# Kernel tuning notes

Measured on AMD Instinct MI355X. Metric: run time of the kernel, lower is better.

Reference implementation:

```python
import math
import jax, jax.numpy as jnp
import numpy as np

B, T = 2, 2048
D_MODEL, D_HEAD = 2048, 128
N_Q, N_KV = 16, 4
QPG = N_Q // N_KV  # queries per kv group
ROPE_BASE = 10000.0
YARN_SCALE = 4.0
ORIG_MAX_LEN = 4096
BETA_FAST, BETA_SLOW = 32.0, 1.0
RMS_EPS = 1.1920929e-07  # torch.finfo(float32).eps (nn.RMSNorm default)


def _yarn_inv_freq():
    inv = 1.0 / ROPE_BASE ** (np.arange(0, D_HEAD, 2, dtype=np.float32) / D_HEAD)
    wavelengths = 2.0 * math.pi / inv
    low_wavelen = ORIG_MAX_LEN / BETA_SLOW
    high_wavelen = ORIG_MAX_LEN / BETA_FAST
    gamma = np.clip((low_wavelen - wavelengths) / (low_wavelen - high_wavelen), 0.0, 1.0)
    return (gamma * inv + (1.0 - gamma) * inv / YARN_SCALE).astype(np.float32)

INV_FREQ = jnp.asarray(_yarn_inv_freq())  # (D_HEAD//2,) constant buffer
MSCALE = 0.1 * math.log(YARN_SCALE) + 1.0
ATTN_SCALE = 1.0 / (MSCALE * math.sqrt(D_HEAD))


def _rms_norm(x, w):
    # normalize over last dim (d_head), learnable per-dim weight
    return x * jax.lax.rsqrt(jnp.mean(x * x, axis=-1, keepdims=True) + RMS_EPS) * w


def _apply_rope(x):
    # x: (..., T, d_head)
    t = jnp.arange(x.shape[-2], dtype=jnp.float32)
    freqs = jnp.outer(t, INV_FREQ)                 # (T, d/2)
    emb = jnp.concatenate([freqs, freqs], axis=-1)  # (T, d)
    cos, sin = jnp.cos(emb), jnp.sin(emb)
    half = x.shape[-1] // 2
    x_rot = jnp.concatenate([-x[..., half:], x[..., :half]], axis=-1)
    return x * cos + x_rot * sin


def setup_inputs() -> dict:
    key = jax.random.key(0)
    ks = jax.random.split(key, 5)
    x = jax.random.normal(ks[0], (B, T, D_MODEL), dtype=jnp.float32)
    w_scale = 0.02
    Wq = jax.random.normal(ks[1], (D_MODEL, N_Q * D_HEAD), dtype=jnp.float32) * w_scale
    Wkv = jax.random.normal(ks[2], (D_MODEL, 2 * N_KV * D_HEAD), dtype=jnp.float32) * w_scale
    Wo = jax.random.normal(ks[3], (N_Q * D_HEAD, D_MODEL), dtype=jnp.float32) * w_scale
    q_norm_w = jnp.ones((D_HEAD,), dtype=jnp.float32)
    k_norm_w = jnp.ones((D_HEAD,), dtype=jnp.float32)
    return {"x": x, "Wq": Wq, "Wkv": Wkv, "Wo": Wo,
            "q_norm_w": q_norm_w, "k_norm_w": k_norm_w}


def reference(x, Wq, Wkv, Wo, q_norm_w, k_norm_w):
    b, t, _ = x.shape
    # projections
    q = (x @ Wq).reshape(b, t, QPG, N_KV, D_HEAD).transpose(0, 2, 3, 1, 4)  # (b,qpg,g,t,d)
    kv = x @ Wkv
    k, v = jnp.split(kv, 2, axis=-1)
    k = k.reshape(b, t, N_KV, D_HEAD).transpose(0, 2, 1, 3)  # (b,g,t,d)
    v = v.reshape(b, t, N_KV, D_HEAD).transpose(0, 2, 1, 3)  # (b,g,t,d)
    # RMSNorm + YaRN RoPE on q,k (math done in float32 as in source)
    q = _apply_rope(_rms_norm(q, q_norm_w))
    k = _apply_rope(_rms_norm(k, k_norm_w))
    # GQA replication: head index h = qpg*N_KV + g (matches source rearrange/reshape)
    q = q.reshape(b, N_Q, t, D_HEAD)
    k = jnp.broadcast_to(k[:, None], (b, QPG, N_KV, t, D_HEAD)).reshape(b, N_Q, t, D_HEAD)
    v = jnp.broadcast_to(v[:, None], (b, QPG, N_KV, t, D_HEAD)).reshape(b, N_Q, t, D_HEAD)
    # causal SDPA with custom scale
    scores = jnp.einsum('bhtd,bhsd->bhts', q, k) * ATTN_SCALE
    causal = jnp.tril(jnp.ones((t, t), dtype=bool))
    scores = jnp.where(causal, scores, jnp.finfo(scores.dtype).min)
    probs = jax.nn.softmax(scores, axis=-1)
    attn = jnp.einsum('bhts,bhsd->bhtd', probs, v)
    out = attn.transpose(0, 2, 1, 3).reshape(b, t, N_Q * D_HEAD)
    return out @ Wo
```

## Files before the change

kernel.cpp:

```cpp
#include <hip/hip_runtime.h>
#include <cmath>

typedef float f32x4 __attribute__((ext_vector_type(4)));
typedef __bf16 bf16x8 __attribute__((ext_vector_type(8)));

#define DEV static __device__ __forceinline__

DEV unsigned short f2bf(float f) {
  unsigned int u = __builtin_bit_cast(unsigned int, f);
  u += 0x7FFFu + ((u >> 16) & 1u);
  return (unsigned short)(u >> 16);
}
DEV float bf2f(unsigned short h) {
  unsigned int u = ((unsigned int)h) << 16;
  return __builtin_bit_cast(float, u);
}
DEV unsigned int cvtpk(float lo, float hi) {
  unsigned int r;
  asm("v_cvt_pk_bf16_f32 %0, %1, %2" : "=v"(r) : "v"(lo), "v"(hi));
  return r;
}
DEV f32x4 mfma16(bf16x8 a, bf16x8 b, f32x4 c) {
  return __builtin_amdgcn_mfma_f32_16x16x32_bf16(a, b, c, 0, 0, 0);
}
DEV void dma16(const void* g, void* l) {
  __builtin_amdgcn_global_load_lds(
      (const __attribute__((address_space(1))) void*)(uintptr_t)g,
      (__attribute__((address_space(3))) void*)(unsigned int)(uintptr_t)l,
      16, 0, 0);
}

constexpr int T_SEQ = 2048;

__global__ __launch_bounds__(256) void prep_all(const float4* __restrict__ in,
                                                ushort* __restrict__ out,
                                                float2* __restrict__ rope,
                                                const float* __restrict__ Wq,
                                                const float* __restrict__ Wkv,
                                                const float* __restrict__ Wo,
                                                ushort* __restrict__ wqkv,
                                                ushort* __restrict__ wot) {
  __shared__ ushort tile[64][65];
  const int bx = blockIdx.x;
  if (bx < 8192) {
    int i = bx * 256 + threadIdx.x;
    float4 v = in[i];
    unsigned int lo = (unsigned int)f2bf(v.x) | ((unsigned int)f2bf(v.y) << 16);
    unsigned int hi = (unsigned int)f2bf(v.z) | ((unsigned int)f2bf(v.w) << 16);
    int row = i >> 9;
    int e = (i * 4) & 2047;
    size_t o = ((size_t)row << 11) + (size_t)(e ^ ((row & 7) << 3));
    *(uint2*)(out + o) = make_uint2(lo, hi);
  } else if (bx < 8704) {
    int gid = (bx - 8192) * 256 + threadIdx.x;
    int t = gid >> 6, i = gid & 63;
    double inv = pow(10000.0, -((double)(2 * i)) / 128.0);
    double wl = 6.283185307179586 / inv;
    double gm = (4096.0 - wl) / (4096.0 - 128.0);
    gm = gm < 0.0 ? 0.0 : (gm > 1.0 ? 1.0 : gm);
    float f = (float)(gm * inv + (1.0 - gm) * inv * 0.25);
    float th = (float)t * f;
    float s, c;
    sincosf(th, &s, &c);
    rope[gid] = make_float2(c, s);
  } else {
    const int l = bx - 8704;
    const int bxl0 = l % 80, by = l / 80;
    const float* src;
    ushort* dst;
    int C, bxl;
    if (bxl0 < 32) {
      src = Wq; dst = wqkv; C = 2048; bxl = bxl0;
    } else if (bxl0 < 48) {
      src = Wkv; dst = wqkv + (size_t)2048 * 2048; C = 1024; bxl = bxl0 - 32;
    } else {
      src = Wo; dst = wot; C = 2048; bxl = bxl0 - 48;
    }
    const int R = 2048;
    int c0 = bxl * 64, r0 = by * 64;
    int j = threadIdx.x & 63, i0 = threadIdx.x >> 6;
#pragma unroll
    for (int ii = 0; ii < 16; ++ii) {
      int i = i0 + ii * 4;
      tile[i][j] = f2bf(src[(size_t)(r0 + i) * C + c0 + j]);
    }
    __syncthreads();
#pragma unroll
    for (int ii = 0; ii < 16; ++ii) {
      int jr = i0 + ii * 4;
      dst[(size_t)(c0 + jr) * R + ((r0 + j) ^ ((jr & 7) << 3))] = tile[j][jr];
    }
  }
}

template <int BM, int BN, int OUT_BF16>
__global__ __launch_bounds__(512) void gemm256(const ushort* __restrict__ A,
                                               const ushort* __restrict__ Bt,
                                               void* __restrict__ Cv,
                                               int M, int N, int K) {
  constexpr int MT = BM / 32;
  constexpr int NT = BN / 64;
  constexpr int NPH = (MT / 4) * (NT / 2);
  constexpr int ADMA = BM / 64;
  constexpr int BDMA = BN / 64;
  __shared__ ushort lA[2][BM * 64];
  __shared__ ushort lB[2][BN * 64];
  const int tid = threadIdx.x, lane = tid & 63, w = tid >> 6;
  const int wm = (w >> 2) * (BM / 2);
  const int wn = (w & 3) * (BN / 4);
  const int m0 = blockIdx.y * BM, n0 = blockIdx.x * BN;

  f32x4 acc[MT][NT] = {};

  const size_t K2 = (size_t)K * 2;
  const char* Ab = (const char*)A + (size_t)m0 * K2;
  const char* Bb = (const char*)Bt + (size_t)n0 * K2;
  const int srb = lane >> 3;
  const int scb = (lane & 7) * 16;

  auto stage = [&](int t, int bi) {
#pragma unroll
    for (int ii = 0; ii < ADMA; ++ii) {
      const int ar = w * (BM / 8) + ii * 8;
      dma16(Ab + (size_t)(ar + srb) * K2 + (size_t)t * 128 + scb,
            (char*)lA[bi] + ar * 128);
    }
#pragma unroll
    for (int ii = 0; ii < BDMA; ++ii) {
      const int br = w * (BN / 8) + ii * 8;
      dma16(Bb + (size_t)(br + srb) * K2 + (size_t)t * 128 + scb,
            (char*)lB[bi] + br * 128);
    }
  };

  stage(0, 0);
  const int nkt = K >> 6;

  for (int t = 0; t < nkt; ++t) {
    const int cur = t & 1;
    if (t + 1 < nkt) {
      stage(t + 1, cur ^ 1);
      if constexpr (ADMA + BDMA == 8)
        asm volatile("s_waitcnt vmcnt(8)" ::: "memory");
      else if constexpr (ADMA + BDMA == 6)
        asm volatile("s_waitcnt vmcnt(6)" ::: "memory");
      else
        asm volatile("s_waitcnt vmcnt(4)" ::: "memory");
    } else {
      asm volatile("s_waitcnt vmcnt(0)" ::: "memory");
    }
    __builtin_amdgcn_s_barrier();
    __builtin_amdgcn_sched_barrier(0);

    const char* lAc = (const char*)lA[cur];
    const char* lBc = (const char*)lB[cur];

#pragma unroll
    for (int ph = 0; ph < NPH; ++ph) {
      const int mb = (ph / (NT / 2)) * 4;
      const int nb = (ph % (NT / 2)) * 2;
#pragma unroll
      for (int kk = 0; kk < 2; ++kk) {
        bf16x8 af[4], bfr[2];
        const int byo = kk * 64 + ((lane >> 4) << 4);
#pragma unroll
        for (int i = 0; i < 4; ++i) {
          int row = wm + (mb + i) * 16 + (lane & 15);
          af[i] = *(const bf16x8*)(lAc + row * 128 + (byo ^ ((row & 7) << 4)));
        }
#pragma unroll
        for (int i = 0; i < 2; ++i) {
          int row = wn + (nb + i) * 16 + (lane & 15);
          bfr[i] = *(const bf16x8*)(lBc + row * 128 + (byo ^ ((row & 7) << 4)));
        }
        __builtin_amdgcn_s_setprio(1);
#pragma unroll
        for (int i = 0; i < 4; ++i)
#pragma unroll
          for (int j = 0; j < 2; ++j)
            acc[mb + i][nb + j] = mfma16(af[i], bfr[j], acc[mb + i][nb + j]);
        __builtin_amdgcn_s_setprio(0);
      }
    }
    __builtin_amdgcn_sched_barrier(0);
    __builtin_amdgcn_s_barrier();
  }

  const int rr = (lane >> 4) << 2;
  const int cc = lane & 15;
  if (OUT_BF16) {
    ushort* C = (ushort*)Cv;
#pragma unroll
    for (int mt = 0; mt < MT; ++mt)
#pragma unroll
      for (int nt = 0; nt < NT; ++nt)
#pragma unroll
        for (int j = 0; j < 4; ++j) {
          int r = m0 + wm + mt * 16 + rr + j;
          int c = n0 + wn + nt * 16 + cc;
          C[(size_t)r * N + c] = f2bf(acc[mt][nt][j]);
        }
  } else {
    float* C = (float*)Cv;
#pragma unroll
    for (int mt = 0; mt < MT; ++mt)
#pragma unroll
      for (int nt = 0; nt < NT; ++nt)
#pragma unroll
        for (int j = 0; j < 4; ++j) {
          int r = m0 + wm + mt * 16 + rr + j;
          int c = n0 + wn + nt * 16 + cc;
          C[(size_t)r * N + c] = acc[mt][nt][j];
        }
  }
}

__global__ __launch_bounds__(256) void normrope_tv(const ushort* __restrict__ qkv,
                                                   const float* __restrict__ qw,
                                                   const float* __restrict__ kw,
                                                   const float2* __restrict__ rope,
                                                   ushort* __restrict__ qout,
                                                   ushort* __restrict__ kout,
                                                   ushort* __restrict__ vt,
                                                   float q_scale) {
  __shared__ ushort tile[64][65];
  const int bx = blockIdx.x;
  if (bx < 20480) {
    const int w = threadIdx.x >> 6, lane = threadIdx.x & 63;
    const int vi = bx * 4 + w;
    const ushort* src;
    const float* wt;
    ushort* dst;
    float extra;
    int t, bb;
    if (vi < 65536) {
      int row = vi >> 4, H = vi & 15;
      bb = row >> 11;
      t = row & 2047;
      src = qkv + (size_t)row * 3072 + H * 128 + lane * 2;
      wt = qw;
      extra = q_scale;
      dst = qout + ((size_t)(bb * 16 + H) * T_SEQ + t) * 128 + lane * 2;
    } else {
      int vi2 = vi - 65536;
      int row = vi2 >> 2, gg = vi2 & 3;
      bb = row >> 11;
      t = row & 2047;
      src = qkv + (size_t)row * 3072 + 2048 + gg * 128 + lane * 2;
      wt = kw;
      extra = 1.f;
      dst = kout + ((size_t)(bb * 4 + gg) * T_SEQ + t) * 128 +
            ((lane * 2) ^ ((t & 7) << 3));
    }
    float x0 = bf2f(src[0]), x1 = bf2f(src[1]);
    float ss = x0 * x0 + x1 * x1;
#pragma unroll
    for (int d = 1; d < 64; d <<= 1) ss += __shfl_xor(ss, d, 64);
    float sc = rsqrtf(ss * (1.f / 128.f) + 1.1920929e-7f);
    float w0 = wt[lane * 2], w1 = wt[lane * 2 + 1];
    float xn0 = x0 * sc * w0, xn1 = x1 * sc * w1;
    float p0 = __shfl_xor(xn0, 32, 64), p1 = __shfl_xor(xn1, 32, 64);
    float r0 = lane < 32 ? -p0 : p0;
    float r1 = lane < 32 ? -p1 : p1;
    int i0 = (lane * 2) & 63;
    float2 cs0 = rope[t * 64 + i0];
    float2 cs1 = rope[t * 64 + i0 + 1];
    float o0 = (xn0 * cs0.x + r0 * cs0.y) * extra;
    float o1 = (xn1 * cs1.x + r1 * cs1.y) * extra;
    unsigned int pkv = (unsigned int)f2bf(o0) | ((unsigned int)f2bf(o1) << 16);
    *(unsigned int*)dst = pkv;
  } else {
    const int l = bx - 20480;
    int t0 = (l & 31) * 64;
    int y = l >> 5;
    int dh = y & 1, bg = y >> 1;
    int bb = bg >> 2, g = bg & 3;
    int j = threadIdx.x & 63, i0 = threadIdx.x >> 6;
#pragma unroll
    for (int ii = 0; ii < 16; ++ii) {
      int i = i0 + ii * 4;
      tile[i][j] = qkv[(size_t)(bb * T_SEQ + t0 + i) * 3072 + 2560 + g * 128 + dh * 64 + j];
    }
    __syncthreads();
#pragma unroll
    for (int ii = 0; ii < 16; ++ii) {
      int jr = i0 + ii * 4;
      vt[((size_t)bg * 128 + dh * 64 + jr) * T_SEQ + ((t0 + j) ^ ((jr & 7) << 3))] = tile[j][jr];
    }
  }
}

__global__ __launch_bounds__(256, 2) void attn_fwd(const ushort* __restrict__ qh,
                                                   const ushort* __restrict__ kh,
                                                   const ushort* __restrict__ vt,
                                                   ushort* __restrict__ o) {
  const int f = blockIdx.x;
  const int half = f >> 8, c = f & 255;
  const int kk = c >> 5, bh = c & 31;
  const int qt = half ? kk : (15 - kk);
  const int b = bh >> 4, H = bh & 15;
  const int g = H & 3;
  const int tid = threadIdx.x, lane = tid & 63, w = tid >> 6;
  const int wrow0 = qt * 128 + w * 32;

  __shared__ ushort lK[2][64 * 128];
  __shared__ ushort lV[2][128 * 64];
  __shared__ ushort lP[4 * 32 * 64];

  bf16x8 qf[2][4];
#pragma unroll
  for (int mt = 0; mt < 2; ++mt) {
    const ushort* qb = qh + ((size_t)(b * 16 + H) * T_SEQ + wrow0 + mt * 16 + (lane & 15)) * 128 +
                       ((lane >> 4) << 3);
#pragma unroll
    for (int kc = 0; kc < 4; ++kc) qf[mt][kc] = *(const bf16x8*)(qb + kc * 32);
  }

  f32x4 oacc[2][8] = {};
  float mrow[2] = {-INFINITY, -INFINITY};
  float lrow[2] = {0.f, 0.f};

  const char* kpl = (const char*)(kh + (size_t)(b * 4 + g) * T_SEQ * 128);
  const char* vpl = (const char*)(vt + (size_t)(b * 4 + g) * 128 * T_SEQ);

  auto stage = [&](int j, int bi) {
#pragma unroll
    for (int ii = 0; ii < 4; ++ii) {
      const int off = w * 4096 + ii * 1024;
      dma16(kpl + (size_t)j * 16384 + off + lane * 16, (char*)lK[bi] + off);
      const int vrow = w * 32 + ii * 8 + (lane >> 3);
      dma16(vpl + (size_t)vrow * (T_SEQ * 2) + j * 128 + (lane & 7) * 16,
            (char*)lV[bi] + off);
    }
  };

  stage(0, 0);

  const int rsel = ((lane >> 4) << 2);

  const int jmax = 2 * qt + 1;
  for (int j = 0; j <= jmax; ++j) {
    const int cur = j & 1;
    if (j < jmax) {
      stage(j + 1, cur ^ 1);
      asm volatile("s_waitcnt vmcnt(8)" ::: "memory");
    } else {
      asm volatile("s_waitcnt vmcnt(0)" ::: "memory");
    }
    __builtin_amdgcn_s_barrier();
    __builtin_amdgcn_sched_barrier(0);

    f32x4 s[2][4];
#pragma unroll
    for (int nt = 0; nt < 4; ++nt) {
      bf16x8 kf[4];
      int krow = nt * 16 + (lane & 15);
#pragma unroll
      for (int kc = 0; kc < 4; ++kc) {
        int byo = kc * 64 + ((lane >> 4) << 4);
        kf[kc] = *(const bf16x8*)((const char*)lK[cur] + krow * 256 + (byo ^ ((krow & 7) << 4)));
      }
#pragma unroll
      for (int mt = 0; mt < 2; ++mt) {
        f32x4 a = {0.f, 0.f, 0.f, 0.f};
#pragma unroll
        for (int kc = 0; kc < 4; ++kc) a = mfma16(kf[kc], qf[mt][kc], a);
        s[mt][nt] = a;
      }
    }

    if (j * 64 + 63 > wrow0) {
#pragma unroll
      for (int mt = 0; mt < 2; ++mt) {
        int qrow = wrow0 + mt * 16 + (lane & 15);
#pragma unroll
        for (int nt = 0; nt < 4; ++nt)
#pragma unroll
          for (int jj = 0; jj < 4; ++jj) {
            int col = j * 64 + nt * 16 + rsel + jj;
            if (col > qrow) s[mt][nt][jj] = -3.0e38f;
          }
      }
    }

    float pmx[2], mn[2];
#pragma unroll
    for (int mt = 0; mt < 2; ++mt) {
      float a0 = fmaxf(fmaxf(s[mt][0][0], s[mt][0][1]), fmaxf(s[mt][0][2], s[mt][0][3]));
      float a1 = fmaxf(fmaxf(s[mt][1][0], s[mt][1][1]), fmaxf(s[mt][1][2], s[mt][1][3]));
      float a2 = fmaxf(fmaxf(s[mt][2][0], s[mt][2][1]), fmaxf(s[mt][2][2], s[mt][2][3]));
      float a3 = fmaxf(fmaxf(s[mt][3][0], s[mt][3][1]), fmaxf(s[mt][3][2], s[mt][3][3]));
      float p = fmaxf(fmaxf(a0, a1), fmaxf(a2, a3));
      p = fmaxf(p, __shfl_xor(p, 16, 64));
      p = fmaxf(p, __shfl_xor(p, 32, 64));
      pmx[mt] = p;
      mn[mt] = mrow[mt];
    }

    bool ok = (pmx[0] <= mrow[0] + 11.5417f) && (pmx[1] <= mrow[1] + 11.5417f);
    if (!__all(ok)) {
#pragma unroll
      for (int mt = 0; mt < 2; ++mt) {
        mn[mt] = fmaxf(mrow[mt], pmx[mt]);
        float rsc = exp2f(mrow[mt] - mn[mt]);
        mrow[mt] = mn[mt];
        lrow[mt] *= rsc;
        float rr0 = __shfl(rsc, rsel + 0, 64);
        float rr1 = __shfl(rsc, rsel + 1, 64);
        float rr2 = __shfl(rsc, rsel + 2, 64);
        float rr3 = __shfl(rsc, rsel + 3, 64);
#pragma unroll
        for (int dt = 0; dt < 8; ++dt) {
          oacc[mt][dt][0] *= rr0; oacc[mt][dt][1] *= rr1;
          oacc[mt][dt][2] *= rr2; oacc[mt][dt][3] *= rr3;
        }
      }
    }

#pragma unroll
    for (int mt = 0; mt < 2; ++mt) {
      float ps = 0.f;
      int prow = mt * 16 + (lane & 15);
      char* pbase = (char*)lP + w * 4096 + prow * 128;
      int swz = (prow & 7) << 4;
#pragma unroll
      for (int nt = 0; nt < 4; ++nt) {
        float p0 = exp2f(s[mt][nt][0] - mn[mt]);
        float p1 = exp2f(s[mt][nt][1] - mn[mt]);
        float p2 = exp2f(s[mt][nt][2] - mn[mt]);
        float p3 = exp2f(s[mt][nt][3] - mn[mt]);
        ps += (p0 + p1) + (p2 + p3);
        int pcb = (nt * 32 + ((lane >> 4) << 3)) ^ swz;
        *(uint2*)(pbase + pcb) = make_uint2(cvtpk(p0, p1), cvtpk(p2, p3));
      }
      ps += __shfl_xor(ps, 16, 64);
      ps += __shfl_xor(ps, 32, 64);
      lrow[mt] += ps;
    }

#pragma unroll
    for (int kc2 = 0; kc2 < 2; ++kc2) {
      bf16x8 pa[2];
#pragma unroll
      for (int mt = 0; mt < 2; ++mt) {
        int prow = mt * 16 + (lane & 15);
        int pbo = kc2 * 64 + ((lane >> 4) << 4);
        pa[mt] = *(const bf16x8*)((char*)lP + w * 4096 + prow * 128 + (pbo ^ ((prow & 7) << 4)));
      }
#pragma unroll
      for (int dt = 0; dt < 8; ++dt) {
        int vrow = dt * 16 + (lane & 15);
        int vbo = kc2 * 64 + ((lane >> 4) << 4);
        bf16x8 vf = *(const bf16x8*)((const char*)lV[cur] + vrow * 128 + (vbo ^ ((vrow & 7) << 4)));
#pragma unroll
        for (int mt = 0; mt < 2; ++mt) oacc[mt][dt] = mfma16(pa[mt], vf, oacc[mt][dt]);
      }
    }

    __builtin_amdgcn_sched_barrier(0);
    __builtin_amdgcn_s_barrier();
  }

#pragma unroll
  for (int mt = 0; mt < 2; ++mt) {
    float linv = 1.f / lrow[mt];
    float iv0 = __shfl(linv, rsel + 0, 64);
    float iv1 = __shfl(linv, rsel + 1, 64);
    float iv2 = __shfl(linv, rsel + 2, 64);
    float iv3 = __shfl(linv, rsel + 3, 64);
    int row = wrow0 + mt * 16 + rsel;
#pragma unroll
    for (int dt = 0; dt < 8; ++dt) {
      int col = H * 128 + dt * 16 + (lane & 15);
      o[(size_t)(b * T_SEQ + row + 0) * 2048 + (col ^ (((row + 0) & 7) << 3))] =
          f2bf(oacc[mt][dt][0] * iv0);
      o[(size_t)(b * T_SEQ + row + 1) * 2048 + (col ^ (((row + 1) & 7) << 3))] =
          f2bf(oacc[mt][dt][1] * iv1);
      o[(size_t)(b * T_SEQ + row + 2) * 2048 + (col ^ (((row + 2) & 7) << 3))] =
          f2bf(oacc[mt][dt][2] * iv2);
      o[(size_t)(b * T_SEQ + row + 3) * 2048 + (col ^ (((row + 3) & 7) << 3))] =
          f2bf(oacc[mt][dt][3] * iv3);
    }
  }
}

extern "C" void kernel_launch(void* const* d_in, const int* in_sizes, int n_in,
                              void* d_out, int out_size, void* d_ws, size_t ws_size,
                              hipStream_t stream) {
  (void)in_sizes; (void)n_in; (void)out_size; (void)ws_size;
  const float* x = (const float*)d_in[0];
  const float* Wq = (const float*)d_in[1];
  const float* Wkv = (const float*)d_in[2];
  const float* Wo = (const float*)d_in[3];
  const float* qnw = (const float*)d_in[4];
  const float* knw = (const float*)d_in[5];
  float* out = (float*)d_out;
  char* ws = (char*)d_ws;

  ushort* xb = (ushort*)(ws);
  ushort* wqkv = (ushort*)(ws + 16777216);
  ushort* wot = (ushort*)(ws + 29360128);
  ushort* qkvraw = (ushort*)(ws + 37748736);
  ushort* kh = (ushort*)(ws + 62914560);
  ushort* vtp = (ushort*)(ws + 67108864);
  float2* rope = (float2*)(ws + 71303168);
  ushort* qh = xb;
  ushort* attnb = qkvraw;

  float attn_scale = 1.0f / ((0.1f * logf(4.0f) + 1.0f) * sqrtf(128.0f));
  float q_scale = attn_scale * 1.44269504f;

  prep_all<<<11264, 256, 0, stream>>>((const float4*)x, xb, rope, Wq, Wkv, Wo, wqkv, wot);
  gemm256<128, 384, 1><<<dim3(8, 32), 512, 0, stream>>>(xb, wqkv, qkvraw, 4096, 3072, 2048);
  normrope_tv<<<20992, 256, 0, stream>>>(qkvraw, qnw, knw, rope, qh, kh, vtp, q_scale);
  attn_fwd<<<512, 256, 0, stream>>>(qh, kh, vtp, attnb);
  gemm256<128, 256, 0><<<dim3(8, 32), 512, 0, stream>>>(attnb, wot, out, 4096, 2048, 2048);
}
```

Before: 201.1 us.

## Interleave next-tile prefetch with MFMA phases and reuse A fragments in GEMM

Restructures the GEMM main loop. The A fragments are read from shared memory once per K-tile and reused across all N phases, instead of being reloaded in every phase. The global-to-LDS copies for the next tile are split across the first two compute phases, with a full vmcnt(0) wait and barrier at the end of each tile. This aims to overlap memory traffic with MFMA work and cut redundant LDS reads, at the cost of extra per-phase barriers and an implicit assumption that MT equals 4.

```diff
diff --git a/kernel.cpp b/kernel.cpp
--- a/kernel.cpp
+++ b/kernel.cpp
@@ -100,9 +100,10 @@
                                                int M, int N, int K) {
   constexpr int MT = BM / 32;
   constexpr int NT = BN / 64;
-  constexpr int NPH = (MT / 4) * (NT / 2);
+  constexpr int NPH = NT / 2;
   constexpr int ADMA = BM / 64;
   constexpr int BDMA = BN / 64;
+  constexpr int BC0 = (BDMA + 1) / 2;
   __shared__ ushort lA[2][BM * 64];
   __shared__ ushort lB[2][BN * 64];
   const int tid = threadIdx.x, lane = tid & 63, w = tid >> 6;
@@ -118,71 +119,81 @@
   const int srb = lane >> 3;
   const int scb = (lane & 7) * 16;
 
-  auto stage = [&](int t, int bi) {
+  auto stageA = [&](int t, int bi) {
 #pragma unroll
     for (int ii = 0; ii < ADMA; ++ii) {
       const int ar = w * (BM / 8) + ii * 8;
       dma16(Ab + (size_t)(ar + srb) * K2 + (size_t)t * 128 + scb,
             (char*)lA[bi] + ar * 128);
     }
-#pragma unroll
-    for (int ii = 0; ii < BDMA; ++ii) {
+  };
+  auto stageB = [&](int t, int bi, int l0, int cnt) {
+    for (int ii = l0; ii < l0 + cnt; ++ii) {
       const int br = w * (BN / 8) + ii * 8;
       dma16(Bb + (size_t)(br + srb) * K2 + (size_t)t * 128 + scb,
             (char*)lB[bi] + br * 128);
     }
   };
 
-  stage(0, 0);
+  stageA(0, 0);
+  stageB(0, 0, 0, BDMA);
   const int nkt = K >> 6;
+
+  asm volatile("s_waitcnt vmcnt(0)" ::: "memory");
+  __builtin_amdgcn_s_barrier();
 
   for (int t = 0; t < nkt; ++t) {
     const int cur = t & 1;
-    if (t + 1 < nkt) {
-      stage(t + 1, cur ^ 1);
-      if constexpr (ADMA + BDMA == 8)
-        asm volatile("s_waitcnt vmcnt(8)" ::: "memory");
-      else if constexpr (ADMA + BDMA == 6)
-        asm volatile("s_waitcnt vmcnt(6)" ::: "memory");
-      else
-        asm volatile("s_waitcnt vmcnt(4)" ::: "memory");
-    } else {
-      asm volatile("s_waitcnt vmcnt(0)" ::: "memory");
-    }
-    __builtin_amdgcn_s_barrier();
-    __builtin_amdgcn_sched_barrier(0);
-
     const char* lAc = (const char*)lA[cur];
     const char* lBc = (const char*)lB[cur];
-
+    const bool pre = (t + 1 < nkt);
+
+    bf16x8 af[2][4];
 #pragma unroll
     for (int ph = 0; ph < NPH; ++ph) {
-      const int mb = (ph / (NT / 2)) * 4;
-      const int nb = (ph % (NT / 2)) * 2;
+      if (ph == 0) {
+#pragma unroll
+        for (int kk = 0; kk < 2; ++kk) {
+          const int byo = kk * 64 + ((lane >> 4) << 4);
+#pragma unroll
+          for (int i = 0; i < 4; ++i) {
+            int row = wm + i * 16 + (lane & 15);
+            af[kk][i] = *(const bf16x8*)(lAc + row * 128 + (byo ^ ((row & 7) << 4)));
+          }
+        }
+      }
+      bf16x8 bfr[2][2];
 #pragma unroll
       for (int kk = 0; kk < 2; ++kk) {
-        bf16x8 af[4], bfr[2];
         const int byo = kk * 64 + ((lane >> 4) << 4);
 #pragma unroll
-        for (int i = 0; i < 4; ++i) {
-          int row = wm + (mb + i) * 16 + (lane & 15);
-          af[i] = *(const bf16x8*)(lAc + row * 128 + (byo ^ ((row & 7) << 4)));
+        for (int i = 0; i < 2; ++i) {
+          int row = wn + (2 * ph + i) * 16 + (lane & 15);
+          bfr[kk][i] = *(const bf16x8*)(lBc + row * 128 + (byo ^ ((row & 7) << 4)));
         }
-#pragma unroll
-        for (int i = 0; i < 2; ++i) {
-          int row = wn + (nb + i) * 16 + (lane & 15);
-          bfr[i] = *(const bf16x8*)(lBc + row * 128 + (byo ^ ((row & 7) << 4)));
+      }
+      if (pre) {
+        if (ph == 0) {
+          stageA(t + 1, cur ^ 1);
+          stageB(t + 1, cur ^ 1, 0, BC0);
+        } else if (ph == 1) {
+          stageB(t + 1, cur ^ 1, BC0, BDMA - BC0);
         }
-        __builtin_amdgcn_s_setprio(1);
+      }
+      __builtin_amdgcn_s_barrier();
+      __builtin_amdgcn_sched_barrier(0);
+      __builtin_amdgcn_s_setprio(1);
+#pragma unroll
+      for (int kk = 0; kk < 2; ++kk)
 #pragma unroll
         for (int i = 0; i < 4; ++i)
 #pragma unroll
           for (int j = 0; j < 2; ++j)
-            acc[mb + i][nb + j] = mfma16(af[i], bfr[j], acc[mb + i][nb + j]);
-        __builtin_amdgcn_s_setprio(0);
-      }
+            acc[i][2 * ph + j] = mfma16(af[kk][i], bfr[kk][j], acc[i][2 * ph + j]);
+      __builtin_amdgcn_s_setprio(0);
     }
     __builtin_amdgcn_sched_barrier(0);
+    asm volatile("s_waitcnt vmcnt(0)" ::: "memory");
     __builtin_amdgcn_s_barrier();
   }
 
```

Measured after the change: 197.5 us. No clear change (-1.7%).
